# Optimization experiments

Hardware: AMD Instinct MI355X
Metric: run time of the kernel (lower is better)

Reference implementation:

```python
import jax, jax.numpy as jnp
import numpy as np

N_NODES = 50000
N_EDGES = 640000
D_IN = 128
D_HID = 256
D_OUT = 128


def _linear_params(key, d_in, d_out):
    kw, kb = jax.random.split(key)
    bound = 1.0 / np.sqrt(d_in)
    W = jax.random.uniform(kw, (d_in, d_out), jnp.float32, -bound, bound)
    b = jax.random.uniform(kb, (d_out,), jnp.float32, -bound, bound)
    return W, b


def setup_inputs() -> dict:
    key = jax.random.key(0)
    ks = jax.random.split(key, 6)
    x = jax.random.normal(ks[0], (N_NODES, D_IN), jnp.float32)
    edge_index = jax.random.randint(ks[1], (2, N_EDGES), 0, N_NODES, jnp.int64)
    W1a, b1a = _linear_params(ks[2], D_IN, D_HID)
    W1b, b1b = _linear_params(ks[3], D_HID, D_HID)
    W2a, b2a = _linear_params(ks[4], D_HID, D_HID)
    W2b, b2b = _linear_params(ks[5], D_HID, D_OUT)
    return {"x": x, "edge_index": edge_index,
            "W1a": W1a, "b1a": b1a, "W1b": W1b, "b1b": b1b,
            "W2a": W2a, "b2a": b2a, "W2b": W2b, "b2b": b2b}


def _gin_conv(x, src, dst, Wa, ba, Wb, bb):
    # sum-aggregate neighbor features: agg[i] = sum_{(j->i) in E} x[j]
    agg = jax.ops.segment_sum(x[src], dst, num_segments=N_NODES)
    h = x + agg  # (1 + eps) * x + agg, eps = 0 (PyG default)
    h = jnp.maximum(h @ Wa + ba, 0.0)  # Linear + ReLU
    return h @ Wb + bb                 # Linear


def reference(x, edge_index, W1a, b1a, W1b, b1b, W2a, b2a, W2b, b2b):
    src, dst = edge_index[0], edge_index[1]
    h = _gin_conv(x, src, dst, W1a, b1a, W1b, b1b)
    h = jnp.maximum(h, 0.0)  # ReLU; dropout is identity in eval mode
    return _gin_conv(h, src, dst, W2a, b2a, W2b, b2b)
```

## Files before the change

### kernel.cpp

```cpp
#include <hip/hip_runtime.h>

#define N_NODES 50000
#define N_EDGES 640000
#define PADROWS 50048
#define SLOTS   48

typedef __attribute__((ext_vector_type(8))) short bf16x8;
typedef __attribute__((ext_vector_type(4))) float f32x4;

__device__ inline ushort rne16(float f) {
    unsigned u = __builtin_bit_cast(unsigned, f);
    unsigned r = u + 0x7fffu + ((u >> 16) & 1u);
    return (ushort)(r >> 16);
}
__device__ inline float b2f(ushort h) {
    return __builtin_bit_cast(float, (unsigned)h << 16);
}

__device__ inline void glds16(const ushort* g, ushort* l) {
    __builtin_amdgcn_global_load_lds(
        (const __attribute__((address_space(1))) void*)g,
        (__attribute__((address_space(3))) void*)l, 16, 0, 0);
}

#define EB  ((N_EDGES + 255) / 256)
#define RB  ((N_NODES * 128 / 4 + 255) / 256)

__global__ __launch_bounds__(256) void prep_kernel(const int* __restrict__ src,
                                                   const int* __restrict__ dst,
                                                   int* __restrict__ cnt,
                                                   ushort* __restrict__ elist,
                                                   const float* __restrict__ W1a,
                                                   const float* __restrict__ W1b,
                                                   const float* __restrict__ W2a,
                                                   const float* __restrict__ W2b,
                                                   ushort* __restrict__ o1a,
                                                   ushort* __restrict__ o1b,
                                                   ushort* __restrict__ o2a,
                                                   ushort* __restrict__ o2b,
                                                   const float* __restrict__ x,
                                                   ushort* __restrict__ xb) {
    __shared__ float tileLds[32][33];
    int blk = blockIdx.x;
    if (blk < EB) {
        int e = blk * 256 + threadIdx.x;
        if (e < N_EDGES) {
            unsigned d = (unsigned)dst[e];
            unsigned s = (unsigned)src[e];
            if (d < N_NODES && s < N_NODES) {
                int pos = atomicAdd(&cnt[d], 1);
                if (pos < SLOTS) elist[(size_t)d * SLOTS + pos] = (ushort)s;
            }
        }
        return;
    }
    blk -= EB;
    if (blk < 192) {
        const float* W; ushort* O; int K, N, tbase;
        if (blk < 32)       { W = W1a; O = o1a; K = 128; N = 256; tbase = 0; }
        else if (blk < 96)  { W = W1b; O = o1b; K = 256; N = 256; tbase = 32; }
        else if (blk < 160) { W = W2a; O = o2a; K = 256; N = 256; tbase = 96; }
        else                { W = W2b; O = o2b; K = 256; N = 128; tbase = 160; }
        int tile = blk - tbase;
        int nt = N >> 5;
        int tk = tile / nt, tn = tile % nt;
        int cc = threadIdx.x & 31, rr0 = threadIdx.x >> 5;
#pragma unroll
        for (int it = 0; it < 4; ++it) {
            int r = rr0 + it * 8;
            tileLds[r][cc] = W[(size_t)(tk * 32 + r) * N + tn * 32 + cc];
        }
        __syncthreads();
#pragma unroll
        for (int it = 0; it < 4; ++it) {
            int r = rr0 + it * 8;
            O[(size_t)(tn * 32 + r) * K + tk * 32 + cc] = rne16(tileLds[cc][r]);
        }
        return;
    }
    blk -= 192;
    int i = blk * 256 + threadIdx.x;
    if (i < N_NODES * 128 / 4) {
        float4 v = ((const float4*)x)[i];
        ushort4 o = make_ushort4(rne16(v.x), rne16(v.y), rne16(v.z), rne16(v.w));
        ((ushort4*)xb)[i] = o;
    }
}

__global__ __launch_bounds__(256) void agg_x(const ushort* __restrict__ xb,
                                             const int* __restrict__ cnt,
                                             const ushort* __restrict__ elist,
                                             ushort* __restrict__ h0b) {
    const int l = threadIdx.x & 31;
    const int node = blockIdx.x * 8 + (threadIdx.x >> 5);
    if (node >= N_NODES) return;
    ushort4 s4 = ((const ushort4*)(xb + (size_t)node * 128))[l];
    float a0 = b2f(s4.x), a1 = b2f(s4.y), a2 = b2f(s4.z), a3 = b2f(s4.w);
    float c0 = 0.f, c1 = 0.f, c2 = 0.f, c3 = 0.f;
    int n = cnt[node]; if (n > SLOTS) n = SLOTS;
    const ushort* el = elist + (size_t)node * SLOTS;
    int i = 0;
    for (; i + 2 <= n; i += 2) {
        int s0 = el[i], s1 = el[i + 1];
        ushort4 v0 = ((const ushort4*)(xb + (size_t)s0 * 128))[l];
        ushort4 v1 = ((const ushort4*)(xb + (size_t)s1 * 128))[l];
        a0 += b2f(v0.x); a1 += b2f(v0.y); a2 += b2f(v0.z); a3 += b2f(v0.w);
        c0 += b2f(v1.x); c1 += b2f(v1.y); c2 += b2f(v1.z); c3 += b2f(v1.w);
    }
    if (i < n) {
        ushort4 v = ((const ushort4*)(xb + (size_t)el[i] * 128))[l];
        a0 += b2f(v.x); a1 += b2f(v.y); a2 += b2f(v.z); a3 += b2f(v.w);
    }
    a0 += c0; a1 += c1; a2 += c2; a3 += c3;
    ushort4 o = make_ushort4(rne16(a0), rne16(a1), rne16(a2), rne16(a3));
    ((ushort4*)(h0b + (size_t)node * 128))[l] = o;
}

__global__ __launch_bounds__(256) void agg_h(const ushort* __restrict__ hBb,
                                             const int* __restrict__ cnt,
                                             const ushort* __restrict__ elist,
                                             ushort* __restrict__ hCb) {
    const int l = threadIdx.x & 63;
    const int node = blockIdx.x * 4 + (threadIdx.x >> 6);
    if (node >= N_NODES) return;
    ushort4 s4 = ((const ushort4*)(hBb + (size_t)node * 256))[l];
    float a0 = b2f(s4.x), a1 = b2f(s4.y), a2 = b2f(s4.z), a3 = b2f(s4.w);
    float c0 = 0.f, c1 = 0.f, c2 = 0.f, c3 = 0.f;
    int n = cnt[node]; if (n > SLOTS) n = SLOTS;
    const ushort* el = elist + (size_t)node * SLOTS;
    int i = 0;
    for (; i + 2 <= n; i += 2) {
        int s0 = el[i], s1 = el[i + 1];
        ushort4 v0 = ((const ushort4*)(hBb + (size_t)s0 * 256))[l];
        ushort4 v1 = ((const ushort4*)(hBb + (size_t)s1 * 256))[l];
        a0 += b2f(v0.x); a1 += b2f(v0.y); a2 += b2f(v0.z); a3 += b2f(v0.w);
        c0 += b2f(v1.x); c1 += b2f(v1.y); c2 += b2f(v1.z); c3 += b2f(v1.w);
    }
    if (i < n) {
        ushort4 v = ((const ushort4*)(hBb + (size_t)el[i] * 256))[l];
        a0 += b2f(v.x); a1 += b2f(v.y); a2 += b2f(v.z); a3 += b2f(v.w);
    }
    a0 += c0; a1 += c1; a2 += c2; a3 += c3;
    ushort4 o = make_ushort4(rne16(a0), rne16(a1), rne16(a2), rne16(a3));
    ((ushort4*)(hCb + (size_t)node * 256))[l] = o;
}


template <int K1, int N2, bool RELU2, bool BF16OUT>
__global__ __launch_bounds__(256, 2) void fused_mlp(const ushort* __restrict__ Ag,
                                                    const ushort* __restrict__ W1g,
                                                    const float* __restrict__ b1,
                                                    const ushort* __restrict__ W2g,
                                                    const float* __restrict__ b2,
                                                    float* __restrict__ Cf,
                                                    ushort* __restrict__ Cb,
                                                    int M) {
    constexpr int NI2 = N2 / 32;
    __shared__ ushort bufA[64 * 64];
    __shared__ ushort bufB[256 * 64];
    __shared__ ushort C1[64 * 256];
    const int tid = threadIdx.x;
    const int lane = tid & 63;
    const int wid = tid >> 6;
    const int wm = wid >> 1, wn = wid & 1;
    const int row0 = blockIdx.x * 64;
    const int stB = lane >> 3;
    const int kel = (((lane & 7) << 4) ^ (stB << 4)) >> 1;

    f32x4 acc1[2][8];
#pragma unroll
    for (int i = 0; i < 2; ++i)
#pragma unroll
        for (int j = 0; j < 8; ++j) acc1[i][j] = (f32x4){0.f, 0.f, 0.f, 0.f};

    for (int k0 = 0; k0 < K1; k0 += 64) {
#pragma unroll
        for (int i = 0; i < 10; ++i) {
            int t = i * 4 + wid;
            if (t < 8) glds16(Ag + (size_t)(row0 + t * 8 + stB) * K1 + k0 + kel, bufA + t * 512);
            else       glds16(W1g + (size_t)((t - 8) * 8 + stB) * K1 + k0 + kel, bufB + (t - 8) * 512);
        }
        __syncthreads();
#pragma unroll
        for (int ki = 0; ki < 2; ++ki) {
            const int kb = ki * 64 + ((lane >> 4) << 4);
            bf16x8 a[2], b[8];
#pragma unroll
            for (int mi = 0; mi < 2; ++mi) {
                int row = wm * 32 + mi * 16 + (lane & 15);
                int off = (row * 128 + kb) ^ ((row & 7) << 4);
                a[mi] = *(const bf16x8*)((const char*)bufA + off);
            }
#pragma unroll
            for (int ni = 0; ni < 8; ++ni) {
                int col = wn * 128 + ni * 16 + (lane & 15);
                int off = (col * 128 + kb) ^ ((col & 7) << 4);
                b[ni] = *(const bf16x8*)((const char*)bufB + off);
            }
#pragma unroll
            for (int mi = 0; mi < 2; ++mi)
#pragma unroll
                for (int ni = 0; ni < 8; ++ni)
                    acc1[mi][ni] = __builtin_amdgcn_mfma_f32_16x16x32_bf16(a[mi], b[ni], acc1[mi][ni], 0, 0, 0);
        }
        __syncthreads();
    }
#pragma unroll
    for (int ni = 0; ni < 8; ++ni) {
        int col = wn * 128 + ni * 16 + (lane & 15);
        float bv = b1[col];
#pragma unroll
        for (int mi = 0; mi < 2; ++mi) {
            int rowb = wm * 32 + mi * 16 + ((lane >> 4) << 2);
            f32x4 av = acc1[mi][ni];
#pragma unroll
            for (int r = 0; r < 4; ++r) {
                int row = rowb + r;
                int off = (row * 512 + col * 2) ^ ((row & 7) << 4);
                *(ushort*)((char*)C1 + off) = rne16(fmaxf(av[r] + bv, 0.f));
            }
        }
    }

    f32x4 acc2[2][NI2];
#pragma unroll
    for (int i = 0; i < 2; ++i)
#pragma unroll
        for (int j = 0; j < NI2; ++j) acc2[i][j] = (f32x4){0.f, 0.f, 0.f, 0.f};

    for (int k0 = 0; k0 < 256; k0 += 64) {
#pragma unroll
        for (int i = 0; i < N2 / 32; ++i) {
            int t = i * 4 + wid;
            glds16(W2g + (size_t)(t * 8 + stB) * 256 + k0 + kel, bufB + t * 512);
        }
        __syncthreads();
#pragma unroll
        for (int ki = 0; ki < 2; ++ki) {
            const int kb = ki * 64 + ((lane >> 4) << 4);
            bf16x8 a[2], b[NI2];
#pragma unroll
            for (int mi = 0; mi < 2; ++mi) {
                int row = wm * 32 + mi * 16 + (lane & 15);
                int off = (row * 512 + k0 * 2 + kb) ^ ((row & 7) << 4);
                a[mi] = *(const bf16x8*)((const char*)C1 + off);
            }
#pragma unroll
            for (int ni = 0; ni < NI2; ++ni) {
                int col = wn * (N2 / 2) + ni * 16 + (lane & 15);
                int off = (col * 128 + kb) ^ ((col & 7) << 4);
                b[ni] = *(const bf16x8*)((const char*)bufB + off);
            }
#pragma unroll
            for (int mi = 0; mi < 2; ++mi)
#pragma unroll
                for (int ni = 0; ni < NI2; ++ni)
                    acc2[mi][ni] = __builtin_amdgcn_mfma_f32_16x16x32_bf16(a[mi], b[ni], acc2[mi][ni], 0, 0, 0);
        }
        __syncthreads();
    }
#pragma unroll
    for (int ni = 0; ni < NI2; ++ni) {
        int col = wn * (N2 / 2) + ni * 16 + (lane & 15);
        float bv = b2[col];
#pragma unroll
        for (int mi = 0; mi < 2; ++mi) {
            int rowb = row0 + wm * 32 + mi * 16 + ((lane >> 4) << 2);
            f32x4 av = acc2[mi][ni];
#pragma unroll
            for (int r = 0; r < 4; ++r) {
                int row = rowb + r;
                if (row < M) {
                    float f = av[r] + bv;
                    if (RELU2) f = fmaxf(f, 0.f);
                    if (BF16OUT) Cb[(size_t)row * N2 + col] = rne16(f);
                    else         Cf[(size_t)row * N2 + col] = f;
                }
            }
        }
    }
}


extern "C" void kernel_launch(void* const* d_in, const int* in_sizes, int n_in,
                              void* d_out, int out_size, void* d_ws, size_t ws_size,
                              hipStream_t stream) {
    const float* x   = (const float*)d_in[0];
    const int*   ei  = (const int*)d_in[1];
    const float* W1a = (const float*)d_in[2];
    const float* b1a = (const float*)d_in[3];
    const float* W1b = (const float*)d_in[4];
    const float* b1b = (const float*)d_in[5];
    const float* W2a = (const float*)d_in[6];
    const float* b2a = (const float*)d_in[7];
    const float* W2b = (const float*)d_in[8];
    const float* b2b = (const float*)d_in[9];
    float* out = (float*)d_out;

    const int* src = ei;
    const int* dst = ei + N_EDGES;

    int* cnt      = (int*)d_ws;
    ushort* elist = (ushort*)(cnt + N_NODES);

    size_t ob = (((size_t)N_NODES * 4 + (size_t)N_NODES * SLOTS * 2) + 255) & ~(size_t)255;
    ushort* w1a = (ushort*)((char*)d_ws + ob);
    ushort* w1b = w1a + 256 * 128;
    ushort* w2a = w1b + 256 * 256;
    ushort* w2b = w2a + 256 * 256;
    char*   wend = (char*)(w2b + 128 * 256);

    size_t fb = ((size_t)(wend - (char*)d_ws) + 255) & ~(size_t)255;
    const size_t P128 = (size_t)PADROWS * 128;
    const size_t P256 = (size_t)PADROWS * 256;
    ushort* xb  = (ushort*)((char*)d_ws + fb);
    ushort* h0b = xb  + P128;
    ushort* hBb = h0b + P128;
    ushort* hCb = hBb + P256;

    hipMemsetAsync(cnt, 0, (size_t)N_NODES * sizeof(int), stream);

    prep_kernel<<<EB + 192 + RB, 256, 0, stream>>>(
        src, dst, cnt, elist, W1a, W1b, W2a, W2b, w1a, w1b, w2a, w2b, x, xb);

    const int gb = PADROWS / 64;
    agg_x<<<(N_NODES + 7) / 8, 256, 0, stream>>>(xb, cnt, elist, h0b);
    fused_mlp<128, 256, true, true><<<gb, 256, 0, stream>>>(
        h0b, w1a, b1a, w1b, b1b, nullptr, hBb, N_NODES);
    agg_h<<<(N_NODES + 3) / 4, 256, 0, stream>>>(hBb, cnt, elist, hCb);
    fused_mlp<256, 128, false, false><<<gb, 256, 0, stream>>>(
        hCb, w2a, b2a, w2b, b2b, out, nullptr, N_NODES);
}
```

Before: 194.0 us.

## Load MLP GEMM operands directly from global memory instead of LDS staging

The fused MLP kernel drops the LDS staging buffers for the A tile and the weights. Each wave now reads its MFMA fragments straight from global memory, relying on L1/L2 for reuse, and only the intermediate C1 tile stays in shared memory. This removes the per-iteration __syncthreads and the LDS footprint, so launch bounds rise to 3 blocks per CU for more occupancy. In exchange, each wave fetches redundantly from global/L2 with 16-byte strided row accesses and gets no explicit software prefetch, which may raise memory latency and traffic.

Result: slower. 255.8 us (+31.8%).

```diff
diff --git a/kernel.cpp b/kernel.cpp
--- a/kernel.cpp
+++ b/kernel.cpp
@@ -15,12 +15,6 @@
 }
 __device__ inline float b2f(ushort h) {
     return __builtin_bit_cast(float, (unsigned)h << 16);
-}
-
-__device__ inline void glds16(const ushort* g, ushort* l) {
-    __builtin_amdgcn_global_load_lds(
-        (const __attribute__((address_space(1))) void*)g,
-        (__attribute__((address_space(3))) void*)l, 16, 0, 0);
 }
 
 #define EB  ((N_EDGES + 255) / 256)
@@ -147,7 +141,7 @@
 
 
 template <int K1, int N2, bool RELU2, bool BF16OUT>
-__global__ __launch_bounds__(256, 2) void fused_mlp(const ushort* __restrict__ Ag,
+__global__ __launch_bounds__(256, 3) void fused_mlp(const ushort* __restrict__ Ag,
                                                     const ushort* __restrict__ W1g,
                                                     const float* __restrict__ b1,
                                                     const ushort* __restrict__ W2g,
@@ -156,16 +150,13 @@
                                                     ushort* __restrict__ Cb,
                                                     int M) {
     constexpr int NI2 = N2 / 32;
-    __shared__ ushort bufA[64 * 64];
-    __shared__ ushort bufB[256 * 64];
     __shared__ ushort C1[64 * 256];
     const int tid = threadIdx.x;
     const int lane = tid & 63;
     const int wid = tid >> 6;
     const int wm = wid >> 1, wn = wid & 1;
     const int row0 = blockIdx.x * 64;
-    const int stB = lane >> 3;
-    const int kel = (((lane & 7) << 4) ^ (stB << 4)) >> 1;
+    const int kf = (lane >> 4) << 3;
 
     f32x4 acc1[2][8];
 #pragma unroll
@@ -173,37 +164,24 @@
 #pragma unroll
         for (int j = 0; j < 8; ++j) acc1[i][j] = (f32x4){0.f, 0.f, 0.f, 0.f};
 
-    for (int k0 = 0; k0 < K1; k0 += 64) {
-#pragma unroll
-        for (int i = 0; i < 10; ++i) {
-            int t = i * 4 + wid;
-            if (t < 8) glds16(Ag + (size_t)(row0 + t * 8 + stB) * K1 + k0 + kel, bufA + t * 512);
-            else       glds16(W1g + (size_t)((t - 8) * 8 + stB) * K1 + k0 + kel, bufB + (t - 8) * 512);
-        }
-        __syncthreads();
-#pragma unroll
-        for (int ki = 0; ki < 2; ++ki) {
-            const int kb = ki * 64 + ((lane >> 4) << 4);
+    {
+        const ushort* arow0 = Ag + (size_t)(row0 + wm * 32 + (lane & 15)) * K1 + kf;
+        const ushort* brow0 = W1g + (size_t)(wn * 128 + (lane & 15)) * K1 + kf;
+#pragma unroll 2
+        for (int k = 0; k < K1; k += 32) {
             bf16x8 a[2], b[8];
 #pragma unroll
-            for (int mi = 0; mi < 2; ++mi) {
-                int row = wm * 32 + mi * 16 + (lane & 15);
-                int off = (row * 128 + kb) ^ ((row & 7) << 4);
-                a[mi] = *(const bf16x8*)((const char*)bufA + off);
-            }
-#pragma unroll
-            for (int ni = 0; ni < 8; ++ni) {
-                int col = wn * 128 + ni * 16 + (lane & 15);
-                int off = (col * 128 + kb) ^ ((col & 7) << 4);
-                b[ni] = *(const bf16x8*)((const char*)bufB + off);
-            }
+            for (int mi = 0; mi < 2; ++mi)
+                a[mi] = *(const bf16x8*)(arow0 + (size_t)mi * 16 * K1 + k);
+#pragma unroll
+            for (int ni = 0; ni < 8; ++ni)
+                b[ni] = *(const bf16x8*)(brow0 + (size_t)ni * 16 * K1 + k);
 #pragma unroll
             for (int mi = 0; mi < 2; ++mi)
 #pragma unroll
                 for (int ni = 0; ni < 8; ++ni)
                     acc1[mi][ni] = __builtin_amdgcn_mfma_f32_16x16x32_bf16(a[mi], b[ni], acc1[mi][ni], 0, 0, 0);
         }
-        __syncthreads();
     }
 #pragma unroll
     for (int ni = 0; ni < 8; ++ni) {
@@ -221,6 +199,7 @@
             }
         }
     }
+    __syncthreads();
 
     f32x4 acc2[2][NI2];
 #pragma unroll
@@ -228,36 +207,26 @@
 #pragma unroll
         for (int j = 0; j < NI2; ++j) acc2[i][j] = (f32x4){0.f, 0.f, 0.f, 0.f};
 
-    for (int k0 = 0; k0 < 256; k0 += 64) {
-#pragma unroll
-        for (int i = 0; i < N2 / 32; ++i) {
-            int t = i * 4 + wid;
-            glds16(W2g + (size_t)(t * 8 + stB) * 256 + k0 + kel, bufB + t * 512);
-        }
-        __syncthreads();
-#pragma unroll
-        for (int ki = 0; ki < 2; ++ki) {
-            const int kb = ki * 64 + ((lane >> 4) << 4);
+    {
+        const ushort* brow0 = W2g + (size_t)(wn * (N2 / 2) + (lane & 15)) * 256 + kf;
+#pragma unroll 2
+        for (int k = 0; k < 256; k += 32) {
             bf16x8 a[2], b[NI2];
 #pragma unroll
             for (int mi = 0; mi < 2; ++mi) {
                 int row = wm * 32 + mi * 16 + (lane & 15);
-                int off = (row * 512 + k0 * 2 + kb) ^ ((row & 7) << 4);
+                int off = (row * 512 + k * 2 + ((lane >> 4) << 4)) ^ ((row & 7) << 4);
                 a[mi] = *(const bf16x8*)((const char*)C1 + off);
             }
 #pragma unroll
-            for (int ni = 0; ni < NI2; ++ni) {
-                int col = wn * (N2 / 2) + ni * 16 + (lane & 15);
-                int off = (col * 128 + kb) ^ ((col & 7) << 4);
-                b[ni] = *(const bf16x8*)((const char*)bufB + off);
-            }
+            for (int ni = 0; ni < NI2; ++ni)
+                b[ni] = *(const bf16x8*)(brow0 + (size_t)ni * 16 * 256 + k);
 #pragma unroll
             for (int mi = 0; mi < 2; ++mi)
 #pragma unroll
                 for (int ni = 0; ni < NI2; ++ni)
                     acc2[mi][ni] = __builtin_amdgcn_mfma_f32_16x16x32_bf16(a[mi], b[ni], acc2[mi][ni], 0, 0, 0);
         }
-        __syncthreads();
     }
 #pragma unroll
     for (int ni = 0; ni < NI2; ++ni) {
```
